# Kernel tuning notes

Hardware: AMD Instinct MI355X
Metric: run time of the kernel (lower is better)

The kernel has to match this reference:

```python
import jax, jax.numpy as jnp
import numpy as np

N_NODES = 50000
IN_CH, HID_CH, OUT_CH = 256, 128, 64
N_EDGES = 800000


def setup_inputs() -> dict:
    key = jax.random.key(0)
    ks = jax.random.split(key, 8)
    x = jax.random.normal(ks[0], (N_NODES, IN_CH), dtype=jnp.float32)
    edge_index = jax.random.randint(ks[1], (2, N_EDGES), 0, N_NODES, dtype=jnp.int64)
    edge_weight = jax.random.uniform(ks[2], (N_EDGES,), dtype=jnp.float32)
    # Glorot-style init for the two GCNConv linear layers (PyG uses glorot init, zero bias)
    W1 = jax.random.normal(ks[3], (IN_CH, HID_CH), dtype=jnp.float32) * (2.0 / (IN_CH + HID_CH)) ** 0.5
    b1 = jnp.zeros((HID_CH,), dtype=jnp.float32)
    W2 = jax.random.normal(ks[4], (HID_CH, OUT_CH), dtype=jnp.float32) * (2.0 / (HID_CH + OUT_CH)) ** 0.5
    b2 = jnp.zeros((OUT_CH,), dtype=jnp.float32)
    return {"x": x, "edge_index": edge_index, "edge_weight": edge_weight,
            "W1": W1, "b1": b1, "W2": W2, "b2": b2}


def _gcn_norm(edge_index, edge_weight, num_nodes):
    # PyG gcn_norm with add_self_loops=True: append self loops (weight 1.0),
    # deg[j] = sum of incoming edge weights, norm_e = deg[src]^-1/2 * w_e * deg[dst]^-1/2
    loop = jnp.arange(num_nodes, dtype=edge_index.dtype)
    row = jnp.concatenate([edge_index[0], loop])  # source nodes
    col = jnp.concatenate([edge_index[1], loop])  # destination nodes
    w = jnp.concatenate([edge_weight, jnp.ones((num_nodes,), dtype=edge_weight.dtype)])
    deg = jax.ops.segment_sum(w, col, num_segments=num_nodes)  # [N]
    deg_inv_sqrt = jnp.where(deg > 0, jax.lax.rsqrt(jnp.where(deg > 0, deg, 1.0)), 0.0)
    norm = deg_inv_sqrt[row] * w * deg_inv_sqrt[col]  # [E+N]
    return row, col, norm


def _gcn_conv(x, W, b, row, col, norm, num_nodes):
    h = x @ W                              # [N, C_out] dense linear first (as in PyG)
    msg = h[row] * norm[:, None]           # gather + per-edge scale: [E+N, C_out]
    out = jax.ops.segment_sum(msg, col, num_segments=num_nodes)  # scatter-add to dst
    return out + b


def reference(x, edge_index, edge_weight, W1, b1, W2, b2):
    num_nodes = x.shape[0]
    row, col, norm = _gcn_norm(edge_index, edge_weight, num_nodes)
    h = _gcn_conv(x, W1, b1, row, col, norm, num_nodes)
    h = jax.nn.relu(h)
    # dropout p=0.2 is identity in eval mode (training=False)
    out = _gcn_conv(h, W2, b2, row, col, norm, num_nodes)
    return out
```

## Files before the change

kernel.cpp:

```cpp
#include <hip/hip_runtime.h>
#include <hip/hip_bf16.h>
#include <math.h>

static constexpr int NNODES = 50000;
static constexpr int NEDGES = 800000;
static constexpr int NBUCK = (NNODES + 255) >> 8;
static constexpr int MAXB = 6144;
static constexpr int GEMM1_BLKS = (NNODES + 63) / 64;
static constexpr int BIN_WGS = (NEDGES + 4095) / 4096;
static constexpr int HSTR = 136;

typedef __attribute__((ext_vector_type(8))) short bf16x8;
typedef __attribute__((ext_vector_type(4))) float f32x4;

__device__ inline short f2bf(float f) {
  union { __hip_bfloat16 h; short s; } u;
  u.h = __float2bfloat16(f);
  return u.s;
}

__device__ inline float bf2f(short s) {
  union { unsigned int u; float f; } u;
  u.u = ((unsigned int)(unsigned short)s) << 16;
  return u.f;
}

__device__ inline void i8x8_to_f32(uint2 v, float* f) {
#pragma unroll
  for (int j = 0; j < 4; ++j) f[j] = (float)(signed char)((v.x >> (8 * j)) & 0xFF);
#pragma unroll
  for (int j = 0; j < 4; ++j) f[4 + j] = (float)(signed char)((v.y >> (8 * j)) & 0xFF);
}


template <int K, int NTOT>
__device__ inline void packW_body(const float* __restrict__ W, short* __restrict__ Wpk, int t) {
  constexpr int KF = K / 32;
  constexpr int NPF = NTOT / 16;
  if (t >= KF * NPF * 64) return;
  int f = t >> 6, l = t & 63;
  int kf = f / NPF, nfb = f % NPF;
  int col = nfb * 16 + (l & 15);
  int krow = kf * 32 + (l >> 4) * 8;
  bf16x8 bv;
#pragma unroll
  for (int i = 0; i < 8; ++i) bv[i] = f2bf(W[(size_t)(krow + i) * NTOT + col]);
  ((bf16x8*)Wpk)[t] = bv;
}

__global__ void setup_kernel(const float* __restrict__ W1, short* __restrict__ Wpk1,
                             const float* __restrict__ W2, short* __restrict__ Wpk2,
                             int* __restrict__ gcur) {
  const int bid = blockIdx.x, tid = threadIdx.x;
  if (bid < 16) {
    packW_body<256, 128>(W1, Wpk1, bid * 256 + tid);
  } else if (bid < 20) {
    packW_body<128, 64>(W2, Wpk2, (bid - 16) * 256 + tid);
  } else {
    if (tid < NBUCK) gcur[tid] = tid * MAXB;
  }
}


__device__ inline void gemm1_wave(const float* __restrict__ X, const short* __restrict__ Wpk,
                                  unsigned char* __restrict__ H, float* __restrict__ sc,
                                  int n, int rowbase, int lane) {
  constexpr int KF = 8;
  constexpr int NF = 8;
  const int lrow = lane & 15;
  const int lgrp = lane >> 4;
  const int nmax = n - 1;
  int r = rowbase + lrow;
  r = r > nmax ? nmax : r;
  const bf16x8* Wf = (const bf16x8*)Wpk;
  f32x4 acc[NF] = {};
#pragma unroll
  for (int ks = 0; ks < KF; ++ks) {
    const float* xp = X + (size_t)r * 256 + ks * 32 + lgrp * 8;
    float4 x0 = *(const float4*)xp;
    float4 x1 = *(const float4*)(xp + 4);
    bf16x8 a;
    a[0] = f2bf(x0.x);
    a[1] = f2bf(x0.y);
    a[2] = f2bf(x0.z);
    a[3] = f2bf(x0.w);
    a[4] = f2bf(x1.x);
    a[5] = f2bf(x1.y);
    a[6] = f2bf(x1.z);
    a[7] = f2bf(x1.w);
#pragma unroll
    for (int nf = 0; nf < NF; ++nf) {
      bf16x8 bfr = Wf[(ks * NF + nf) * 64 + lane];
      acc[nf] = __builtin_amdgcn_mfma_f32_16x16x32_bf16(a, bfr, acc[nf], 0, 0, 0);
    }
  }
#pragma unroll
  for (int rr = 0; rr < 4; ++rr) {
    float m = 0.f;
#pragma unroll
    for (int nf = 0; nf < NF; ++nf) m = fmaxf(m, fabsf(acc[nf][rr]));
#pragma unroll
    for (int mask = 1; mask <= 8; mask <<= 1) m = fmaxf(m, __shfl_xor(m, mask));
    const int r2 = rowbase + lgrp * 4 + rr;
    const float inv = (m > 0.f) ? 127.f / m : 0.f;
    if (r2 < n) {
      if (lrow == 0) sc[r2] = m * (1.f / 127.f);
#pragma unroll
      for (int nf = 0; nf < NF; ++nf) {
        int qv = (int)rintf(acc[nf][rr] * inv);
        qv = qv > 127 ? 127 : (qv < -127 ? -127 : qv);
        H[(size_t)r2 * 128 + nf * 16 + lrow] = (unsigned char)(signed char)qv;
      }
    }
  }
}

__global__ __launch_bounds__(256) void fused1_kernel(
    const float* __restrict__ x, const short* __restrict__ Wpk1,
    unsigned char* __restrict__ h1, float* __restrict__ sc1, int n,
    const int* __restrict__ row, const int* __restrict__ col, const float* __restrict__ w,
    int* __restrict__ gcur, int2* __restrict__ binned, int e_cnt) {
  __shared__ int rcnt[NBUCK];
  __shared__ int rcur[NBUCK];
  __shared__ int gbase[NBUCK];
  const int tid = threadIdx.x;
  if ((int)blockIdx.x < GEMM1_BLKS) {
    const int rowbase = blockIdx.x * 64 + (tid >> 6) * 16;
    gemm1_wave(x, Wpk1, h1, sc1, n, rowbase, tid & 63);
    return;
  }
  const int wg = blockIdx.x - GEMM1_BLKS;
  for (int b = tid; b < NBUCK; b += 256) {
    rcnt[b] = 0;
    rcur[b] = 0;
  }
  __syncthreads();
  const int base = wg * 4096;
  int srcs[16], dsts[16];
  float ws_[16];
#pragma unroll
  for (int j = 0; j < 16; ++j) {
    int idx = base + tid + 256 * j;
    if (idx < e_cnt) {
      srcs[j] = row[idx];
      dsts[j] = col[idx];
      ws_[j] = w[idx];
      atomicAdd(&rcnt[dsts[j] >> 8], 1);
    } else {
      dsts[j] = -1;
    }
  }
  __syncthreads();
  for (int b = tid; b < NBUCK; b += 256)
    if (rcnt[b] > 0) gbase[b] = atomicAdd(&gcur[b], rcnt[b]);
  __syncthreads();
#pragma unroll
  for (int j = 0; j < 16; ++j) {
    if (dsts[j] >= 0) {
      int b = dsts[j] >> 8;
      int dl = dsts[j] & 255;
      int pos = gbase[b] + atomicAdd(&rcur[b], 1);
      binned[pos] = make_int2((dl << 16) | srcs[j], __float_as_int(ws_[j]));
    }
  }
}


__global__ __launch_bounds__(256) void bdeg_kernel(const int2* __restrict__ binned,
                                                   const int* __restrict__ gcur,
                                                   float* __restrict__ dinv,
                                                   int* __restrict__ cntg,
                                                   int* __restrict__ bbase, int n) {
  const int b = blockIdx.x, tid = threadIdx.x;
  if (b == NBUCK) {
    __shared__ int buf[256];
    int v = (tid < NBUCK) ? gcur[tid] - tid * MAXB : 0;
    buf[tid] = v;
    __syncthreads();
    for (int off = 1; off < 256; off <<= 1) {
      int t = (tid >= off) ? buf[tid - off] : 0;
      __syncthreads();
      buf[tid] += t;
      __syncthreads();
    }
    if (tid < NBUCK) bbase[tid] = buf[tid] - v;
    return;
  }
  __shared__ float degf[256];
  __shared__ int cnt[256];
  degf[tid] = 0.f;
  cnt[tid] = 0;
  __syncthreads();
  const int bcnt = gcur[b] - b * MAXB;
  const int2* bp = binned + (size_t)b * MAXB;
  for (int i = tid; i < bcnt; i += 256) {
    int2 e = bp[i];
    int dl = (e.x >> 16) & 255;
    atomicAdd(&degf[dl], __int_as_float(e.y));
    atomicAdd(&cnt[dl], 1);
  }
  __syncthreads();
  int node = b * 256 + tid;
  if (node < n) {
    dinv[node] = 1.0f / sqrtf(degf[tid] + 1.0f);
    cntg[node] = cnt[tid];
  }
}


__global__ __launch_bounds__(256) void csrfill_kernel(
    const int2* __restrict__ binned, const int* __restrict__ gcur,
    const int* __restrict__ bbase, const float* __restrict__ dinv,
    const int* __restrict__ cntg, int* __restrict__ start,
    unsigned int* __restrict__ csr, int n) {
  __shared__ float dvL[256];
  __shared__ int cur[256];
  __shared__ int buf[256];
  const int b = blockIdx.x, tid = threadIdx.x;
  const int node = b * 256 + tid;
  int c = (node < n) ? cntg[node] : 0;
  dvL[tid] = (node < n) ? dinv[node] : 0.f;
  buf[tid] = c;
  __syncthreads();
  for (int off = 1; off < 256; off <<= 1) {
    int t = (tid >= off) ? buf[tid - off] : 0;
    __syncthreads();
    buf[tid] += t;
    __syncthreads();
  }
  int localstart = buf[tid] - c;
  const int gb = bbase[b];
  if (node < n) start[node] = gb + localstart;
  cur[tid] = localstart;
  __syncthreads();
  const int bcnt = gcur[b] - b * MAXB;
  const int2* bp = binned + (size_t)b * MAXB;
  for (int i = tid; i < bcnt; i += 256) {
    int2 e = bp[i];
    int src = e.x & 0xFFFF;
    int dl = (e.x >> 16) & 255;
    float nrm = dinv[src] * __int_as_float(e.y) * dvL[dl];
    int pos = gb + atomicAdd(&cur[dl], 1);
    csr[pos] = (unsigned int)src | ((unsigned int)(unsigned short)f2bf(nrm) << 16);
  }
}


__global__ __launch_bounds__(256) void glayer1_kernel(
    const unsigned char* __restrict__ h, const float* __restrict__ sc,
    const float* __restrict__ dinv, const float* __restrict__ b,
    const int* __restrict__ start, const unsigned int* __restrict__ csr,
    const short* __restrict__ Wpk2, unsigned char* __restrict__ h2,
    float* __restrict__ sc2, int n, int e_cnt) {
  __shared__ short hbuf[16 * HSTR];
  __shared__ float rmax[16][4];
  const int tid = threadIdx.x;
  const int q = tid & 15;
  const int g = tid >> 4;
  const int rowbase = blockIdx.x * 16;
  const int d = rowbase + g;

  {
    float s = dinv[d];
    s = s * s * sc[d];
    float f[8];
    i8x8_to_f32(*(const uint2*)(h + (size_t)d * 128 + q * 8), f);
    float a0[8], a1[8], a2[8], a3[8];
#pragma unroll
    for (int j = 0; j < 8; ++j) {
      a0[j] = f[j] * s + b[q * 8 + j];
      a1[j] = 0.f;
      a2[j] = 0.f;
      a3[j] = 0.f;
    }
    const int k0 = start[d];
    const int k1 = (d + 1 < n) ? start[d + 1] : e_cnt;
    int k = k0;
    for (; k + 4 <= k1; k += 4) {
      unsigned int e0 = csr[k];
      unsigned int e1 = csr[k + 1];
      unsigned int e2 = csr[k + 2];
      unsigned int e3 = csr[k + 3];
      const int s0 = e0 & 0xFFFF, s1 = e1 & 0xFFFF, s2 = e2 & 0xFFFF, s3 = e3 & 0xFFFF;
      uint2 v0 = *(const uint2*)(h + (size_t)s0 * 128 + q * 8);
      uint2 v1 = *(const uint2*)(h + (size_t)s1 * 128 + q * 8);
      uint2 v2 = *(const uint2*)(h + (size_t)s2 * 128 + q * 8);
      uint2 v3 = *(const uint2*)(h + (size_t)s3 * 128 + q * 8);
      float n0 = bf2f((short)(e0 >> 16)) * sc[s0];
      float n1 = bf2f((short)(e1 >> 16)) * sc[s1];
      float n2 = bf2f((short)(e2 >> 16)) * sc[s2];
      float n3 = bf2f((short)(e3 >> 16)) * sc[s3];
      i8x8_to_f32(v0, f);
#pragma unroll
      for (int j = 0; j < 8; ++j) a0[j] += f[j] * n0;
      i8x8_to_f32(v1, f);
#pragma unroll
      for (int j = 0; j < 8; ++j) a1[j] += f[j] * n1;
      i8x8_to_f32(v2, f);
#pragma unroll
      for (int j = 0; j < 8; ++j) a2[j] += f[j] * n2;
      i8x8_to_f32(v3, f);
#pragma unroll
      for (int j = 0; j < 8; ++j) a3[j] += f[j] * n3;
    }
    for (; k < k1; ++k) {
      unsigned int e = csr[k];
      const int s0 = e & 0xFFFF;
      float nv = bf2f((short)(e >> 16)) * sc[s0];
      i8x8_to_f32(*(const uint2*)(h + (size_t)s0 * 128 + q * 8), f);
#pragma unroll
      for (int j = 0; j < 8; ++j) a0[j] += f[j] * nv;
    }
    bf16x8 ov;
#pragma unroll
    for (int j = 0; j < 8; ++j) {
      float v = (a0[j] + a1[j]) + (a2[j] + a3[j]);
      ov[j] = f2bf(fmaxf(v, 0.f));
    }
    *(bf16x8*)&hbuf[g * HSTR + q * 8] = ov;
  }
  __syncthreads();

  {
    const int lane = tid & 63;
    const int wave = tid >> 6;
    const int lrow = lane & 15;
    const int lgrp = lane >> 4;
    const bf16x8* Wf = (const bf16x8*)Wpk2;
    f32x4 acc = {};
#pragma unroll
    for (int ks = 0; ks < 4; ++ks) {
      bf16x8 a = *(const bf16x8*)&hbuf[lrow * HSTR + ks * 32 + lgrp * 8];
      bf16x8 bfr = Wf[(ks * 4 + wave) * 64 + lane];
      acc = __builtin_amdgcn_mfma_f32_16x16x32_bf16(a, bfr, acc, 0, 0, 0);
    }
    float rm[4];
#pragma unroll
    for (int rr = 0; rr < 4; ++rr) {
      float m = fabsf(acc[rr]);
#pragma unroll
      for (int mask = 1; mask <= 8; mask <<= 1) m = fmaxf(m, __shfl_xor(m, mask));
      rm[rr] = m;
    }
    if (lrow == 0) {
#pragma unroll
      for (int rr = 0; rr < 4; ++rr) rmax[lgrp * 4 + rr][wave] = rm[rr];
    }
    __syncthreads();
#pragma unroll
    for (int rr = 0; rr < 4; ++rr) {
      const int rowl = lgrp * 4 + rr;
      const int r2 = rowbase + rowl;
      float m = fmaxf(fmaxf(rmax[rowl][0], rmax[rowl][1]),
                      fmaxf(rmax[rowl][2], rmax[rowl][3]));
      const float inv = (m > 0.f) ? 127.f / m : 0.f;
      if (wave == 0 && lrow == 0) sc2[r2] = m * (1.f / 127.f);
      int qv = (int)rintf(acc[rr] * inv);
      qv = qv > 127 ? 127 : (qv < -127 ? -127 : qv);
      h2[(size_t)r2 * 64 + wave * 16 + lrow] = (unsigned char)(signed char)qv;
    }
  }
}


template <int CH, int TPN, bool RELU, bool OUT_BF16>
__global__ __launch_bounds__(256) void gatherq_kernel(
    const unsigned char* __restrict__ h, const float* __restrict__ sc,
    const float* __restrict__ dinv, const float* __restrict__ b,
    const int* __restrict__ start, const unsigned int* __restrict__ csr,
    void* __restrict__ outp, int n, int e_cnt) {
  constexpr int NPB = 256 / TPN;
  const int tid = threadIdx.x;
  const int q = tid % TPN;
  const int g = tid / TPN;
  const int d = blockIdx.x * NPB + g;
  if (d >= n) return;
  float s = dinv[d];
  s = s * s * sc[d];
  float f[8];
  i8x8_to_f32(*(const uint2*)(h + (size_t)d * CH + q * 8), f);
  float a0[8], a1[8], a2[8], a3[8];
#pragma unroll
  for (int j = 0; j < 8; ++j) {
    a0[j] = f[j] * s + b[q * 8 + j];
    a1[j] = 0.f;
    a2[j] = 0.f;
    a3[j] = 0.f;
  }
  const int k0 = start[d];
  const int k1 = (d + 1 < n) ? start[d + 1] : e_cnt;
  int k = k0;
  for (; k + 4 <= k1; k += 4) {
    unsigned int e0 = csr[k];
    unsigned int e1 = csr[k + 1];
    unsigned int e2 = csr[k + 2];
    unsigned int e3 = csr[k + 3];
    const int s0 = e0 & 0xFFFF, s1 = e1 & 0xFFFF, s2 = e2 & 0xFFFF, s3 = e3 & 0xFFFF;
    uint2 v0 = *(const uint2*)(h + (size_t)s0 * CH + q * 8);
    uint2 v1 = *(const uint2*)(h + (size_t)s1 * CH + q * 8);
    uint2 v2 = *(const uint2*)(h + (size_t)s2 * CH + q * 8);
    uint2 v3 = *(const uint2*)(h + (size_t)s3 * CH + q * 8);
    float n0 = bf2f((short)(e0 >> 16)) * sc[s0];
    float n1 = bf2f((short)(e1 >> 16)) * sc[s1];
    float n2 = bf2f((short)(e2 >> 16)) * sc[s2];
    float n3 = bf2f((short)(e3 >> 16)) * sc[s3];
    i8x8_to_f32(v0, f);
#pragma unroll
    for (int j = 0; j < 8; ++j) a0[j] += f[j] * n0;
    i8x8_to_f32(v1, f);
#pragma unroll
    for (int j = 0; j < 8; ++j) a1[j] += f[j] * n1;
    i8x8_to_f32(v2, f);
#pragma unroll
    for (int j = 0; j < 8; ++j) a2[j] += f[j] * n2;
    i8x8_to_f32(v3, f);
#pragma unroll
    for (int j = 0; j < 8; ++j) a3[j] += f[j] * n3;
  }
  for (; k < k1; ++k) {
    unsigned int e = csr[k];
    const int s0 = e & 0xFFFF;
    float nv = bf2f((short)(e >> 16)) * sc[s0];
    i8x8_to_f32(*(const uint2*)(h + (size_t)s0 * CH + q * 8), f);
#pragma unroll
    for (int j = 0; j < 8; ++j) a0[j] += f[j] * nv;
  }
#pragma unroll
  for (int j = 0; j < 8; ++j) a0[j] += (a1[j] + a2[j]) + a3[j];
  if (RELU) {
#pragma unroll
    for (int j = 0; j < 8; ++j) a0[j] = fmaxf(a0[j], 0.f);
  }
  if (OUT_BF16) {
    bf16x8 ov;
#pragma unroll
    for (int j = 0; j < 8; ++j) ov[j] = f2bf(a0[j]);
    *(bf16x8*)((short*)outp + (size_t)d * CH + q * 8) = ov;
  } else {
    float4* op = (float4*)outp + ((size_t)d * CH + q * 8) / 4;
    op[0] = make_float4(a0[0], a0[1], a0[2], a0[3]);
    op[1] = make_float4(a0[4], a0[5], a0[6], a0[7]);
  }
}


extern "C" void kernel_launch(void* const* d_in, const int* in_sizes, int n_in,
                              void* d_out, int out_size, void* d_ws, size_t ws_size,
                              hipStream_t stream) {
  const float* x = (const float*)d_in[0];
  const int* ei = (const int*)d_in[1];
  const float* ew = (const float*)d_in[2];
  const float* W1 = (const float*)d_in[3];
  const float* b1 = (const float*)d_in[4];
  const float* W2 = (const float*)d_in[5];
  const float* b2 = (const float*)d_in[6];
  float* outp = (float*)d_out;

  const int N = NNODES, E = NEDGES;
  const int* rowp = ei;
  const int* colp = ei + E;

  char* wsb = (char*)d_ws;
  int2* binned = (int2*)wsb;        wsb += (size_t)NBUCK * MAXB * 8;
  unsigned int* csr = (unsigned int*)wsb;  wsb += (size_t)E * 4;
  unsigned char* h1 = (unsigned char*)wsb; wsb += (size_t)N * 128;
  unsigned char* h2 = (unsigned char*)wsb; wsb += (size_t)N * 64;
  short* Wpk1 = (short*)wsb;        wsb += (size_t)256 * 128 * 2;
  short* Wpk2 = (short*)wsb;        wsb += (size_t)128 * 64 * 2;
  float* sc1 = (float*)wsb;         wsb += (size_t)N * 4;
  float* sc2 = (float*)wsb;         wsb += (size_t)N * 4;
  float* dinv = (float*)wsb;        wsb += (size_t)N * 4;
  int* start = (int*)wsb;           wsb += (size_t)N * 4;
  int* cntg = (int*)wsb;            wsb += (size_t)N * 4;
  int* gcur = (int*)wsb;            wsb += (size_t)NBUCK * 4;
  int* bbase = (int*)wsb;           wsb += (size_t)NBUCK * 4;

  setup_kernel<<<21, 256, 0, stream>>>(W1, Wpk1, W2, Wpk2, gcur);

  fused1_kernel<<<GEMM1_BLKS + BIN_WGS, 256, 0, stream>>>(x, Wpk1, h1, sc1, N, rowp, colp,
                                                          ew, gcur, binned, E);

  bdeg_kernel<<<NBUCK + 1, 256, 0, stream>>>(binned, gcur, dinv, cntg, bbase, N);
  csrfill_kernel<<<NBUCK, 256, 0, stream>>>(binned, gcur, bbase, dinv, cntg, start, csr, N);

  glayer1_kernel<<<N / 16, 256, 0, stream>>>(h1, sc1, dinv, b1, start, csr, Wpk2, h2, sc2,
                                             N, E);

  gatherq_kernel<64, 8, false, false><<<(N + 31) / 32, 256, 0, stream>>>(
      h2, sc2, dinv, b2, start, csr, outp, N, E);
}
```

Measured before the change: 92.41 us.

## Merge degree and CSR-fill kernels by factoring GCN normalization out of edges

```diff
diff --git a/kernel.cpp b/kernel.cpp
--- a/kernel.cpp
+++ b/kernel.cpp
@@ -166,88 +166,73 @@
 }
 
 
-__global__ __launch_bounds__(256) void bdeg_kernel(const int2* __restrict__ binned,
-                                                   const int* __restrict__ gcur,
-                                                   float* __restrict__ dinv,
-                                                   int* __restrict__ cntg,
-                                                   int* __restrict__ bbase, int n) {
-  const int b = blockIdx.x, tid = threadIdx.x;
-  if (b == NBUCK) {
-    __shared__ int buf[256];
-    int v = (tid < NBUCK) ? gcur[tid] - tid * MAXB : 0;
-    buf[tid] = v;
-    __syncthreads();
-    for (int off = 1; off < 256; off <<= 1) {
-      int t = (tid >= off) ? buf[tid - off] : 0;
-      __syncthreads();
-      buf[tid] += t;
-      __syncthreads();
-    }
-    if (tid < NBUCK) bbase[tid] = buf[tid] - v;
-    return;
-  }
+__global__ __launch_bounds__(256) void csrbuild_kernel(
+    const int2* __restrict__ binned, const int* __restrict__ gcur,
+    const float* __restrict__ sc1, float* __restrict__ dinv, float* __restrict__ scd1,
+    int* __restrict__ start, unsigned int* __restrict__ csr, int n) {
+  __shared__ int2 ebuf[MAXB];
   __shared__ float degf[256];
   __shared__ int cnt[256];
-  degf[tid] = 0.f;
-  cnt[tid] = 0;
-  __syncthreads();
+  __shared__ int sbuf[256];
+  const int tid = threadIdx.x;
+  const int role = blockIdx.x & 1;
+  const int b = blockIdx.x >> 1;
   const int bcnt = gcur[b] - b * MAXB;
   const int2* bp = binned + (size_t)b * MAXB;
+  const int node = b * 256 + tid;
+
+  if (role == 0) {
+    degf[tid] = 0.f;
+    __syncthreads();
+    for (int i = tid; i < bcnt; i += 256) {
+      int2 e = bp[i];
+      atomicAdd(&degf[(e.x >> 16) & 255], __int_as_float(e.y));
+    }
+    __syncthreads();
+    if (node < n) {
+      float dv = 1.0f / sqrtf(degf[tid] + 1.0f);
+      dinv[node] = dv;
+      scd1[node] = sc1[node] * dv;
+    }
+    return;
+  }
+
+  cnt[tid] = 0;
+  for (int i = tid; i < bcnt; i += 256) ebuf[i] = bp[i];
+  __syncthreads();
+  for (int i = tid; i < bcnt; i += 256) atomicAdd(&cnt[(ebuf[i].x >> 16) & 255], 1);
+  sbuf[tid] = (tid < b) ? (gcur[tid] - tid * MAXB) : 0;
+  __syncthreads();
+  for (int off = 128; off > 0; off >>= 1) {
+    if (tid < off) sbuf[tid] += sbuf[tid + off];
+    __syncthreads();
+  }
+  const int gb = sbuf[0];
+  __syncthreads();
+  sbuf[tid] = cnt[tid];
+  __syncthreads();
+  for (int off = 1; off < 256; off <<= 1) {
+    int t = (tid >= off) ? sbuf[tid - off] : 0;
+    __syncthreads();
+    sbuf[tid] += t;
+    __syncthreads();
+  }
+  const int localstart = sbuf[tid] - cnt[tid];
+  if (node < n) start[node] = gb + localstart;
+  cnt[tid] = localstart;
+  __syncthreads();
   for (int i = tid; i < bcnt; i += 256) {
-    int2 e = bp[i];
+    int2 e = ebuf[i];
     int dl = (e.x >> 16) & 255;
-    atomicAdd(&degf[dl], __int_as_float(e.y));
-    atomicAdd(&cnt[dl], 1);
-  }
-  __syncthreads();
-  int node = b * 256 + tid;
-  if (node < n) {
-    dinv[node] = 1.0f / sqrtf(degf[tid] + 1.0f);
-    cntg[node] = cnt[tid];
-  }
-}
-
-
-__global__ __launch_bounds__(256) void csrfill_kernel(
-    const int2* __restrict__ binned, const int* __restrict__ gcur,
-    const int* __restrict__ bbase, const float* __restrict__ dinv,
-    const int* __restrict__ cntg, int* __restrict__ start,
-    unsigned int* __restrict__ csr, int n) {
-  __shared__ float dvL[256];
-  __shared__ int cur[256];
-  __shared__ int buf[256];
-  const int b = blockIdx.x, tid = threadIdx.x;
-  const int node = b * 256 + tid;
-  int c = (node < n) ? cntg[node] : 0;
-  dvL[tid] = (node < n) ? dinv[node] : 0.f;
-  buf[tid] = c;
-  __syncthreads();
-  for (int off = 1; off < 256; off <<= 1) {
-    int t = (tid >= off) ? buf[tid - off] : 0;
-    __syncthreads();
-    buf[tid] += t;
-    __syncthreads();
-  }
-  int localstart = buf[tid] - c;
-  const int gb = bbase[b];
-  if (node < n) start[node] = gb + localstart;
-  cur[tid] = localstart;
-  __syncthreads();
-  const int bcnt = gcur[b] - b * MAXB;
-  const int2* bp = binned + (size_t)b * MAXB;
-  for (int i = tid; i < bcnt; i += 256) {
-    int2 e = bp[i];
-    int src = e.x & 0xFFFF;
-    int dl = (e.x >> 16) & 255;
-    float nrm = dinv[src] * __int_as_float(e.y) * dvL[dl];
-    int pos = gb + atomicAdd(&cur[dl], 1);
-    csr[pos] = (unsigned int)src | ((unsigned int)(unsigned short)f2bf(nrm) << 16);
+    int pos = gb + atomicAdd(&cnt[dl], 1);
+    csr[pos] = (unsigned int)(e.x & 0xFFFF) |
+               ((unsigned int)(unsigned short)f2bf(__int_as_float(e.y)) << 16);
   }
 }
 
 
 __global__ __launch_bounds__(256) void glayer1_kernel(
-    const unsigned char* __restrict__ h, const float* __restrict__ sc,
+    const unsigned char* __restrict__ h, const float* __restrict__ scd,
     const float* __restrict__ dinv, const float* __restrict__ b,
     const int* __restrict__ start, const unsigned int* __restrict__ csr,
     const short* __restrict__ Wpk2, unsigned char* __restrict__ h2,
@@ -261,14 +246,14 @@
   const int d = rowbase + g;
 
   {
-    float s = dinv[d];
-    s = s * s * sc[d];
+    const float dvd = dinv[d];
+    const float sself = scd[d];
     float f[8];
     i8x8_to_f32(*(const uint2*)(h + (size_t)d * 128 + q * 8), f);
     float a0[8], a1[8], a2[8], a3[8];
 #pragma unroll
     for (int j = 0; j < 8; ++j) {
-      a0[j] = f[j] * s + b[q * 8 + j];
+      a0[j] = f[j] * sself;
       a1[j] = 0.f;
       a2[j] = 0.f;
       a3[j] = 0.f;
@@ -286,10 +271,10 @@
       uint2 v1 = *(const uint2*)(h + (size_t)s1 * 128 + q * 8);
       uint2 v2 = *(const uint2*)(h + (size_t)s2 * 128 + q * 8);
       uint2 v3 = *(const uint2*)(h + (size_t)s3 * 128 + q * 8);
-      float n0 = bf2f((short)(e0 >> 16)) * sc[s0];
-      float n1 = bf2f((short)(e1 >> 16)) * sc[s1];
-      float n2 = bf2f((short)(e2 >> 16)) * sc[s2];
-      float n3 = bf2f((short)(e3 >> 16)) * sc[s3];
+      float n0 = bf2f((short)(e0 >> 16)) * scd[s0];
+      float n1 = bf2f((short)(e1 >> 16)) * scd[s1];
+      float n2 = bf2f((short)(e2 >> 16)) * scd[s2];
+      float n3 = bf2f((short)(e3 >> 16)) * scd[s3];
       i8x8_to_f32(v0, f);
 #pragma unroll
       for (int j = 0; j < 8; ++j) a0[j] += f[j] * n0;
@@ -306,7 +291,7 @@
     for (; k < k1; ++k) {
       unsigned int e = csr[k];
       const int s0 = e & 0xFFFF;
-      float nv = bf2f((short)(e >> 16)) * sc[s0];
+      float nv = bf2f((short)(e >> 16)) * scd[s0];
       i8x8_to_f32(*(const uint2*)(h + (size_t)s0 * 128 + q * 8), f);
 #pragma unroll
       for (int j = 0; j < 8; ++j) a0[j] += f[j] * nv;
@@ -314,7 +299,7 @@
     bf16x8 ov;
 #pragma unroll
     for (int j = 0; j < 8; ++j) {
-      float v = (a0[j] + a1[j]) + (a2[j] + a3[j]);
+      float v = ((a0[j] + a1[j]) + (a2[j] + a3[j])) * dvd + b[q * 8 + j];
       ov[j] = f2bf(fmaxf(v, 0.f));
     }
     *(bf16x8*)&hbuf[g * HSTR + q * 8] = ov;
@@ -354,7 +339,7 @@
       float m = fmaxf(fmaxf(rmax[rowl][0], rmax[rowl][1]),
                       fmaxf(rmax[rowl][2], rmax[rowl][3]));
       const float inv = (m > 0.f) ? 127.f / m : 0.f;
-      if (wave == 0 && lrow == 0) sc2[r2] = m * (1.f / 127.f);
+      if (wave == 0 && lrow == 0) sc2[r2] = m * (1.f / 127.f) * dinv[r2];
       int qv = (int)rintf(acc[rr] * inv);
       qv = qv > 127 ? 127 : (qv < -127 ? -127 : qv);
       h2[(size_t)r2 * 64 + wave * 16 + lrow] = (unsigned char)(signed char)qv;
@@ -363,26 +348,26 @@
 }
 
 
-template <int CH, int TPN, bool RELU, bool OUT_BF16>
+template <int CH, int TPN>
 __global__ __launch_bounds__(256) void gatherq_kernel(
-    const unsigned char* __restrict__ h, const float* __restrict__ sc,
+    const unsigned char* __restrict__ h, const float* __restrict__ scd,
     const float* __restrict__ dinv, const float* __restrict__ b,
     const int* __restrict__ start, const unsigned int* __restrict__ csr,
-    void* __restrict__ outp, int n, int e_cnt) {
+    float* __restrict__ outp, int n, int e_cnt) {
   constexpr int NPB = 256 / TPN;
   const int tid = threadIdx.x;
   const int q = tid % TPN;
   const int g = tid / TPN;
   const int d = blockIdx.x * NPB + g;
   if (d >= n) return;
-  float s = dinv[d];
-  s = s * s * sc[d];
+  const float dvd = dinv[d];
+  const float sself = scd[d];
   float f[8];
   i8x8_to_f32(*(const uint2*)(h + (size_t)d * CH + q * 8), f);
   float a0[8], a1[8], a2[8], a3[8];
 #pragma unroll
   for (int j = 0; j < 8; ++j) {
-    a0[j] = f[j] * s + b[q * 8 + j];
+    a0[j] = f[j] * sself;
     a1[j] = 0.f;
     a2[j] = 0.f;
     a3[j] = 0.f;
@@ -400,10 +385,10 @@
     uint2 v1 = *(const uint2*)(h + (size_t)s1 * CH + q * 8);
     uint2 v2 = *(const uint2*)(h + (size_t)s2 * CH + q * 8);
     uint2 v3 = *(const uint2*)(h + (size_t)s3 * CH + q * 8);
-    float n0 = bf2f((short)(e0 >> 16)) * sc[s0];
-    float n1 = bf2f((short)(e1 >> 16)) * sc[s1];
-    float n2 = bf2f((short)(e2 >> 16)) * sc[s2];
-    float n3 = bf2f((short)(e3 >> 16)) * sc[s3];
+    float n0 = bf2f((short)(e0 >> 16)) * scd[s0];
+    float n1 = bf2f((short)(e1 >> 16)) * scd[s1];
+    float n2 = bf2f((short)(e2 >> 16)) * scd[s2];
+    float n3 = bf2f((short)(e3 >> 16)) * scd[s3];
     i8x8_to_f32(v0, f);
 #pragma unroll
     for (int j = 0; j < 8; ++j) a0[j] += f[j] * n0;
@@ -420,27 +405,18 @@
   for (; k < k1; ++k) {
     unsigned int e = csr[k];
     const int s0 = e & 0xFFFF;
-    float nv = bf2f((short)(e >> 16)) * sc[s0];
+    float nv = bf2f((short)(e >> 16)) * scd[s0];
     i8x8_to_f32(*(const uint2*)(h + (size_t)s0 * CH + q * 8), f);
 #pragma unroll
     for (int j = 0; j < 8; ++j) a0[j] += f[j] * nv;
   }
-#pragma unroll
-  for (int j = 0; j < 8; ++j) a0[j] += (a1[j] + a2[j]) + a3[j];
-  if (RELU) {
-#pragma unroll
-    for (int j = 0; j < 8; ++j) a0[j] = fmaxf(a0[j], 0.f);
-  }
-  if (OUT_BF16) {
-    bf16x8 ov;
-#pragma unroll
-    for (int j = 0; j < 8; ++j) ov[j] = f2bf(a0[j]);
-    *(bf16x8*)((short*)outp + (size_t)d * CH + q * 8) = ov;
-  } else {
-    float4* op = (float4*)outp + ((size_t)d * CH + q * 8) / 4;
-    op[0] = make_float4(a0[0], a0[1], a0[2], a0[3]);
-    op[1] = make_float4(a0[4], a0[5], a0[6], a0[7]);
-  }
+  float out[8];
+#pragma unroll
+  for (int j = 0; j < 8; ++j)
+    out[j] = ((a0[j] + a1[j]) + (a2[j] + a3[j])) * dvd + b[q * 8 + j];
+  float4* op = (float4*)outp + ((size_t)d * CH + q * 8) / 4;
+  op[0] = make_float4(out[0], out[1], out[2], out[3]);
+  op[1] = make_float4(out[4], out[5], out[6], out[7]);
 }
 
 
@@ -468,24 +444,23 @@
   short* Wpk1 = (short*)wsb;        wsb += (size_t)256 * 128 * 2;
   short* Wpk2 = (short*)wsb;        wsb += (size_t)128 * 64 * 2;
   float* sc1 = (float*)wsb;         wsb += (size_t)N * 4;
+  float* scd1 = (float*)wsb;        wsb += (size_t)N * 4;
   float* sc2 = (float*)wsb;         wsb += (size_t)N * 4;
   float* dinv = (float*)wsb;        wsb += (size_t)N * 4;
   int* start = (int*)wsb;           wsb += (size_t)N * 4;
-  int* cntg = (int*)wsb;            wsb += (size_t)N * 4;
   int* gcur = (int*)wsb;            wsb += (size_t)NBUCK * 4;
-  int* bbase = (int*)wsb;           wsb += (size_t)NBUCK * 4;
 
   setup_kernel<<<21, 256, 0, stream>>>(W1, Wpk1, W2, Wpk2, gcur);
 
   fused1_kernel<<<GEMM1_BLKS + BIN_WGS, 256, 0, stream>>>(x, Wpk1, h1, sc1, N, rowp, colp,
                                                           ew, gcur, binned, E);
 
-  bdeg_kernel<<<NBUCK + 1, 256, 0, stream>>>(binned, gcur, dinv, cntg, bbase, N);
-  csrfill_kernel<<<NBUCK, 256, 0, stream>>>(binned, gcur, bbase, dinv, cntg, start, csr, N);
-
-  glayer1_kernel<<<N / 16, 256, 0, stream>>>(h1, sc1, dinv, b1, start, csr, Wpk2, h2, sc2,
+  csrbuild_kernel<<<2 * NBUCK, 256, 0, stream>>>(binned, gcur, sc1, dinv, scd1, start,
+                                                 csr, N);
+
+  glayer1_kernel<<<N / 16, 256, 0, stream>>>(h1, scd1, dinv, b1, start, csr, Wpk2, h2, sc2,
                                              N, E);
 
-  gatherq_kernel<64, 8, false, false><<<(N + 31) / 32, 256, 0, stream>>>(
-      h2, sc2, dinv, b2, start, csr, outp, N, E);
-}
+  gatherq_kernel<64, 8><<<(N + 31) / 32, 256, 0, stream>>>(h2, sc2, dinv, b2, start, csr,
+                                                           outp, N, E);
+}
```

Result: no change. 91.86 us, median of 2 (-0.6%).
